# Kernel tuning notes

Measured on AMD Instinct MI355X. Metric: run time of the kernel, lower is better.

The kernel has to match this reference:

```python
import jax, jax.numpy as jnp
import numpy as np

B, L, D = 4, 2048, 1024
H, KD, VD = 16, 64, 64
EPS = 1e-5


def setup_inputs() -> dict:
    key = jax.random.key(0)
    ks = jax.random.split(key, 12)
    s_in = 1.0 / np.sqrt(D)
    s_out = 1.0 / np.sqrt(H * VD)
    return {
        "queries": jax.random.normal(ks[0], (B, L, D), dtype=jnp.float32),
        "Wq": jax.random.uniform(ks[1], (D, H * KD), jnp.float32, -s_in, s_in),
        "bq": jax.random.uniform(ks[2], (H * KD,), jnp.float32, -s_in, s_in),
        "Wk": jax.random.uniform(ks[3], (D, H * KD), jnp.float32, -s_in, s_in),
        "bk": jax.random.uniform(ks[4], (H * KD,), jnp.float32, -s_in, s_in),
        "Wv": jax.random.uniform(ks[5], (D, H * VD), jnp.float32, -s_in, s_in),
        "bv": jax.random.uniform(ks[6], (H * VD,), jnp.float32, -s_in, s_in),
        "Wo": jax.random.uniform(ks[7], (H * VD, D), jnp.float32, -s_out, s_out),
        "bo": jax.random.uniform(ks[8], (D,), jnp.float32, -s_out, s_out),
        "gamma": jnp.ones((D,), jnp.float32),
        "beta": jnp.zeros((D,), jnp.float32),
    }


def reference(queries, Wq, bq, Wk, bk, Wv, bv, Wo, bo, gamma, beta):
    # QKV projections -> [B, L, H, head_dim]
    q = (queries @ Wq + bq).reshape(B, L, H, KD)
    k = (queries @ Wk + bk).reshape(B, L, H, KD)
    v = (queries @ Wv + bv).reshape(B, L, H, VD)
    # scaled dot-product attention per head: scores [B, H, Lq, Lk]
    scores = jnp.einsum("bqhd,bkhd->bhqk", q, k) / np.sqrt(KD).astype(np.float32)
    attn = jax.nn.softmax(scores, axis=-1)
    out = jnp.einsum("bhqk,bkhd->bqhd", attn, v).reshape(B, L, H * VD)
    # out projection (dropout is identity in eval), residual + LayerNorm
    res = out @ Wo + bo + queries
    mu = jnp.mean(res, axis=-1, keepdims=True)
    var = jnp.var(res, axis=-1, keepdims=True)
    return (res - mu) / jnp.sqrt(var + EPS) * gamma + beta
```

## Files before the change

kernel.cpp:

```cpp
#include <hip/hip_runtime.h>
#include <hip/hip_bf16.h>

#define BATCH 4
#define SEQ   2048
#define DIM   1024
#define NHEAD 16
#define HDIM  64
#define EPS_LN 1e-5f
#define QSCALE 0.18033688011112042f

typedef __attribute__((ext_vector_type(8))) short short8;
typedef __attribute__((ext_vector_type(4))) float f32x4;

__device__ __forceinline__ unsigned short f2bf(float x) {
    __hip_bfloat16 h = __float2bfloat16(x);
    return *reinterpret_cast<unsigned short*>(&h);
}
__device__ __forceinline__ unsigned int pack2bf(float a, float b) {
    __hip_bfloat162 h = __float22bfloat162_rn(float2{a, b});
    return *reinterpret_cast<unsigned int*>(&h);
}

__device__ __forceinline__ void gl_lds16(const void* g, void* l) {
    __builtin_amdgcn_global_load_lds(
        (const __attribute__((address_space(1))) unsigned int*)g,
        (__attribute__((address_space(3))) unsigned int*)l,
        16, 0, 0);
}

__global__ __launch_bounds__(256) void prep_kernel(const float* __restrict__ W0,
                                                   const float* __restrict__ W1,
                                                   const float* __restrict__ W2,
                                                   const float* __restrict__ W3,
                                                   const float* __restrict__ queries,
                                                   unsigned short* __restrict__ Wqkvt,
                                                   unsigned short* __restrict__ Wot,
                                                   unsigned short* __restrict__ qout)
{
    const int z = blockIdx.z;
    const int t = threadIdx.x;

    if (z == 4) {
        const int nthr = 16 * 16 * 256;
        int i = (blockIdx.y * 16 + blockIdx.x) * 256 + t;
        for (int it = 0; it < (BATCH * SEQ * DIM / 4) / nthr; it++, i += nthr) {
            float4 v = ((const float4*)queries)[i];
            ushort4 u;
            u.x = f2bf(v.x); u.y = f2bf(v.y); u.z = f2bf(v.z); u.w = f2bf(v.w);
            ((ushort4*)qout)[i] = u;
        }
        return;
    }

    __shared__ float Ts[64][65];
    const float* W = (z == 0) ? W0 : (z == 1) ? W1 : (z == 2) ? W2 : W3;
    unsigned short* Wt = (z == 3) ? Wot : (Wqkvt + (size_t)z * DIM * DIM);

    const int k0 = blockIdx.y * 64, n0 = blockIdx.x * 64;
    const int lr = t >> 2, lq = t & 3;

#pragma unroll
    for (int i = 0; i < 4; i++) {
        float4 v = *(const float4*)(W + (size_t)(k0 + lr) * DIM + n0 + (lq * 4 + i) * 4);
        Ts[lr][(lq * 4 + i) * 4 + 0] = v.x;
        Ts[lr][(lq * 4 + i) * 4 + 1] = v.y;
        Ts[lr][(lq * 4 + i) * 4 + 2] = v.z;
        Ts[lr][(lq * 4 + i) * 4 + 3] = v.w;
    }
    __syncthreads();
#pragma unroll
    for (int i = 0; i < 4; i++) {
        const int c = lq * 16 + i * 4;
        ushort4 u;
        u.x = f2bf(Ts[c + 0][lr]);
        u.y = f2bf(Ts[c + 1][lr]);
        u.z = f2bf(Ts[c + 2][lr]);
        u.w = f2bf(Ts[c + 3][lr]);
        *(ushort4*)(Wt + (size_t)(n0 + lr) * DIM + k0 + c) = u;
    }
}

__global__ __launch_bounds__(256) void gemm_qkv(const unsigned short* __restrict__ A,
                                                const unsigned short* __restrict__ Bt,
                                                const float* __restrict__ bq,
                                                const float* __restrict__ bk,
                                                const float* __restrict__ bv,
                                                unsigned short* __restrict__ Qbf,
                                                unsigned short* __restrict__ Kbf,
                                                unsigned short* __restrict__ Vtb)
{
    __shared__ __attribute__((aligned(16))) unsigned short As[128 * 32];
    __shared__ __attribute__((aligned(16))) unsigned short Bs[128 * 32];

    const int tid = threadIdx.x;
    const int w = tid >> 6, lane = tid & 63;
    const int col = lane & 15, quad = lane >> 4;
    const int wm = (w >> 1) * 64, wn = (w & 1) * 64;
    const int m0 = blockIdx.y * 128, n0 = blockIdx.x * 128;

    f32x4 acc[4][4] = {};
    const int srow = tid >> 2, sc4 = tid & 3;

    for (int k0 = 0; k0 < DIM; k0 += 32) {
        __syncthreads();
#pragma unroll
        for (int it = 0; it < 2; it++) {
            gl_lds16(A  + (size_t)(m0 + srow + it * 64) * DIM + k0 + sc4 * 8,
                     (char*)As + w * 1024 + it * 4096);
            gl_lds16(Bt + (size_t)(n0 + srow + it * 64) * DIM + k0 + sc4 * 8,
                     (char*)Bs + w * 1024 + it * 4096);
        }
        __syncthreads();

        short8 af[4], bf[4];
#pragma unroll
        for (int mt = 0; mt < 4; mt++) af[mt] = *(short8*)&As[(wm + mt * 16 + col) * 32 + quad * 8];
#pragma unroll
        for (int nt = 0; nt < 4; nt++) bf[nt] = *(short8*)&Bs[(wn + nt * 16 + col) * 32 + quad * 8];

#pragma unroll
        for (int mt = 0; mt < 4; mt++)
#pragma unroll
            for (int nt = 0; nt < 4; nt++)
                acc[mt][nt] = __builtin_amdgcn_mfma_f32_16x16x32_bf16(af[mt], bf[nt], acc[mt][nt], 0, 0, 0);
    }

    const int sector = n0 >> 10;
    const float* bias = (sector == 0) ? bq : (sector == 1) ? bk : bv;

#pragma unroll
    for (int nt = 0; nt < 4; nt++) {
        const int n = n0 + wn + nt * 16 + col;
        const int nloc = n - (sector << 10);
        const float bvv = bias[nloc];
#pragma unroll
        for (int mt = 0; mt < 4; mt++) {
            const int mbase = m0 + wm + mt * 16 + quad * 4;
            if (sector == 0) {
#pragma unroll
                for (int r = 0; r < 4; r++)
                    Qbf[(size_t)(mbase + r) * DIM + nloc] = f2bf((acc[mt][nt][r] + bvv) * QSCALE);
            } else if (sector == 1) {
#pragma unroll
                for (int r = 0; r < 4; r++)
                    Kbf[(size_t)(mbase + r) * DIM + nloc] = f2bf(acc[mt][nt][r] + bvv);
            } else {
                const int h = nloc >> 6, d = nloc & 63;
                const int b = mbase >> 11, l = mbase & 2047;
                ushort4 u;
                u.x = f2bf(acc[mt][nt][0] + bvv);
                u.y = f2bf(acc[mt][nt][1] + bvv);
                u.z = f2bf(acc[mt][nt][2] + bvv);
                u.w = f2bf(acc[mt][nt][3] + bvv);
                *(ushort4*)(Vtb + ((size_t)((b * NHEAD + h) * HDIM + d)) * SEQ + l) = u;
            }
        }
    }
}

__global__ __launch_bounds__(256) void gemm_out(const unsigned short* __restrict__ A,
                                                const unsigned short* __restrict__ Bt,
                                                const float* __restrict__ bias,
                                                const float* __restrict__ resid,
                                                float* __restrict__ Cout)
{
    __shared__ __attribute__((aligned(16))) unsigned short As[128 * 32];
    __shared__ __attribute__((aligned(16))) unsigned short Bs[128 * 32];

    const int tid = threadIdx.x;
    const int w = tid >> 6, lane = tid & 63;
    const int col = lane & 15, quad = lane >> 4;
    const int wm = (w >> 1) * 64, wn = (w & 1) * 64;
    const int m0 = blockIdx.y * 128, n0 = blockIdx.x * 128;

    f32x4 acc[4][4] = {};
    const int srow = tid >> 2, sc4 = tid & 3;

    for (int k0 = 0; k0 < DIM; k0 += 32) {
        __syncthreads();
#pragma unroll
        for (int it = 0; it < 2; it++) {
            gl_lds16(A  + (size_t)(m0 + srow + it * 64) * DIM + k0 + sc4 * 8,
                     (char*)As + w * 1024 + it * 4096);
            gl_lds16(Bt + (size_t)(n0 + srow + it * 64) * DIM + k0 + sc4 * 8,
                     (char*)Bs + w * 1024 + it * 4096);
        }
        __syncthreads();

        short8 af[4], bf[4];
#pragma unroll
        for (int mt = 0; mt < 4; mt++) af[mt] = *(short8*)&As[(wm + mt * 16 + col) * 32 + quad * 8];
#pragma unroll
        for (int nt = 0; nt < 4; nt++) bf[nt] = *(short8*)&Bs[(wn + nt * 16 + col) * 32 + quad * 8];

#pragma unroll
        for (int mt = 0; mt < 4; mt++)
#pragma unroll
            for (int nt = 0; nt < 4; nt++)
                acc[mt][nt] = __builtin_amdgcn_mfma_f32_16x16x32_bf16(af[mt], bf[nt], acc[mt][nt], 0, 0, 0);
    }

#pragma unroll
    for (int nt = 0; nt < 4; nt++) {
        const int n = n0 + wn + nt * 16 + col;
        const float bvv = bias[n];
#pragma unroll
        for (int mt = 0; mt < 4; mt++) {
            const int mbase = m0 + wm + mt * 16 + quad * 4;
#pragma unroll
            for (int r = 0; r < 4; r++) {
                const size_t off = (size_t)(mbase + r) * DIM + n;
                Cout[off] = acc[mt][nt][r] + bvv + resid[off];
            }
        }
    }
}

#define KP 72
__global__ __launch_bounds__(256) void attn_mfma(const unsigned short* __restrict__ Qb,
                                                 const unsigned short* __restrict__ Kb,
                                                 const unsigned short* __restrict__ Vt,
                                                 unsigned short* __restrict__ Ob)
{
    __shared__ __attribute__((aligned(16))) unsigned short Ks[64 * KP];
    __shared__ __attribute__((aligned(16))) unsigned short Vs[64 * KP];
    __shared__ __attribute__((aligned(16))) unsigned short Ps[4][32 * KP];

    const int tid = threadIdx.x;
    const int w = tid >> 6, lane = tid & 63;
    const int col = lane & 15, quad = lane >> 4;

    const int bh  = blockIdx.x & 63;
    const int qt_ = blockIdx.x >> 6;
    const int b   = bh >> 4;
    const int h   = bh & 15;

    const int q0 = qt_ * 128 + w * 32;

    short8 qf[2][2];
#pragma unroll
    for (int qt = 0; qt < 2; qt++) {
        const size_t base = ((size_t)(b * SEQ) + q0 + qt * 16 + col) * DIM + h * HDIM + quad * 8;
        qf[qt][0] = *(const short8*)(Qb + base);
        qf[qt][1] = *(const short8*)(Qb + base + 32);
    }

    short8 onesf;
    {
        const short v = (col == 0) ? (short)0x3F80 : (short)0;
        onesf = short8{v, v, v, v, v, v, v, v};
    }

    f32x4 o[4][2] = {};
    f32x4 od[2]   = {};

    const size_t kbase0 = ((size_t)(b * SEQ)) * DIM + h * HDIM;
    const size_t vbase0 = ((size_t)((b * NHEAD + h) * HDIM)) * SEQ;

    const int srow = tid >> 3, sc = tid & 7;
    unsigned short* Pw = Ps[w];

    for (int kt = 0; kt < SEQ / 64; kt++) {
        __syncthreads();
#pragma unroll
        for (int it = 0; it < 2; it++) {
            const int row = srow + it * 32;
            *(int4*)&Ks[row * KP + sc * 8] = *(const int4*)(Kb + kbase0 + (size_t)(kt * 64 + row) * DIM + sc * 8);
            *(int4*)&Vs[row * KP + sc * 8] = *(const int4*)(Vt + vbase0 + (size_t)row * SEQ + kt * 64 + sc * 8);
        }
        __syncthreads();

#pragma unroll
        for (int nt = 0; nt < 4; nt++) {
            short8 kf0 = *(short8*)&Ks[(nt * 16 + col) * KP + quad * 8];
            short8 kf1 = *(short8*)&Ks[(nt * 16 + col) * KP + quad * 8 + 32];
#pragma unroll
            for (int qt = 0; qt < 2; qt++) {
                f32x4 s = {};
                s = __builtin_amdgcn_mfma_f32_16x16x32_bf16(kf0, qf[qt][0], s, 0, 0, 0);
                s = __builtin_amdgcn_mfma_f32_16x16x32_bf16(kf1, qf[qt][1], s, 0, 0, 0);
                const float p0 = __builtin_amdgcn_exp2f(s[0]);
                const float p1 = __builtin_amdgcn_exp2f(s[1]);
                const float p2 = __builtin_amdgcn_exp2f(s[2]);
                const float p3 = __builtin_amdgcn_exp2f(s[3]);
                uint2 pk;
                pk.x = pack2bf(p0, p1);
                pk.y = pack2bf(p2, p3);
                *(uint2*)&Pw[(qt * 16 + col) * KP + nt * 16 + quad * 4] = pk;
            }
        }

        short8 pf[2][2];
#pragma unroll
        for (int qt = 0; qt < 2; qt++) {
            pf[qt][0] = *(short8*)&Pw[(qt * 16 + col) * KP + quad * 8];
            pf[qt][1] = *(short8*)&Pw[(qt * 16 + col) * KP + quad * 8 + 32];
        }

#pragma unroll
        for (int qt = 0; qt < 2; qt++) {
            od[qt] = __builtin_amdgcn_mfma_f32_16x16x32_bf16(onesf, pf[qt][0], od[qt], 0, 0, 0);
            od[qt] = __builtin_amdgcn_mfma_f32_16x16x32_bf16(onesf, pf[qt][1], od[qt], 0, 0, 0);
        }

#pragma unroll
        for (int mt = 0; mt < 4; mt++) {
            short8 vf0 = *(short8*)&Vs[(mt * 16 + col) * KP + quad * 8];
            short8 vf1 = *(short8*)&Vs[(mt * 16 + col) * KP + quad * 8 + 32];
#pragma unroll
            for (int qt = 0; qt < 2; qt++) {
                o[mt][qt] = __builtin_amdgcn_mfma_f32_16x16x32_bf16(vf0, pf[qt][0], o[mt][qt], 0, 0, 0);
                o[mt][qt] = __builtin_amdgcn_mfma_f32_16x16x32_bf16(vf1, pf[qt][1], o[mt][qt], 0, 0, 0);
            }
        }
    }

#pragma unroll
    for (int qt = 0; qt < 2; qt++) {
        const float den = __shfl(od[qt][0], col);
        const float inv = 1.f / den;
        const size_t rowoff = ((size_t)(b * SEQ) + q0 + qt * 16 + col) * DIM + h * HDIM;
#pragma unroll
        for (int mt = 0; mt < 4; mt++) {
            ushort4 u;
            u.x = f2bf(o[mt][qt][0] * inv);
            u.y = f2bf(o[mt][qt][1] * inv);
            u.z = f2bf(o[mt][qt][2] * inv);
            u.w = f2bf(o[mt][qt][3] * inv);
            *(ushort4*)(Ob + rowoff + mt * 16 + quad * 4) = u;
        }
    }
}

__global__ __launch_bounds__(256) void layernorm_kernel(float* __restrict__ res,
                                                        const float* __restrict__ gamma,
                                                        const float* __restrict__ beta)
{
    const int tid = threadIdx.x;
    const int row = blockIdx.x;
    float4 xv = ((const float4*)(res + (size_t)row * DIM))[tid];

    float s  = xv.x + xv.y + xv.z + xv.w;
    float sq = xv.x * xv.x + xv.y * xv.y + xv.z * xv.z + xv.w * xv.w;
#pragma unroll
    for (int off = 32; off; off >>= 1) {
        s  += __shfl_xor(s, off);
        sq += __shfl_xor(sq, off);
    }
    __shared__ float sm[8];
    const int w = tid >> 6, lane = tid & 63;
    if (lane == 0) { sm[w] = s; sm[4 + w] = sq; }
    __syncthreads();
    const float st  = sm[0] + sm[1] + sm[2] + sm[3];
    const float sqt = sm[4] + sm[5] + sm[6] + sm[7];
    const float mu   = st * (1.f / DIM);
    const float var  = sqt * (1.f / DIM) - mu * mu;
    const float rstd = rsqrtf(var + EPS_LN);

    float4 g  = ((const float4*)gamma)[tid];
    float4 be = ((const float4*)beta)[tid];
    float4 o;
    o.x = (xv.x - mu) * rstd * g.x + be.x;
    o.y = (xv.y - mu) * rstd * g.y + be.y;
    o.z = (xv.z - mu) * rstd * g.z + be.z;
    o.w = (xv.w - mu) * rstd * g.w + be.w;
    ((float4*)(res + (size_t)row * DIM))[tid] = o;
}

extern "C" void kernel_launch(void* const* d_in, const int* in_sizes, int n_in,
                              void* d_out, int out_size, void* d_ws, size_t ws_size,
                              hipStream_t stream)
{
    const float* queries = (const float*)d_in[0];
    const float* Wq = (const float*)d_in[1];
    const float* bq = (const float*)d_in[2];
    const float* Wk = (const float*)d_in[3];
    const float* bk = (const float*)d_in[4];
    const float* Wv = (const float*)d_in[5];
    const float* bv = (const float*)d_in[6];
    const float* Wo = (const float*)d_in[7];
    const float* bo = (const float*)d_in[8];
    const float* gamma = (const float*)d_in[9];
    const float* beta  = (const float*)d_in[10];
    float* outp = (float*)d_out;

    const int M = BATCH * SEQ;
    const size_t BUF = (size_t)M * DIM;
    const size_t WSZ = (size_t)DIM * DIM;

    unsigned short* w0  = (unsigned short*)d_ws;
    unsigned short* qin = w0;
    unsigned short* Qbf = w0 + BUF;
    unsigned short* Kbf = w0 + 2 * BUF;
    unsigned short* Vtb = w0 + 3 * BUF;
    unsigned short* Wqkvt = w0 + 4 * BUF;
    unsigned short* Wot   = Wqkvt + 3 * WSZ;
    unsigned short* Obf = qin;

    dim3 blk(256);

    dim3 pgrid(DIM / 64, DIM / 64, 5);
    prep_kernel<<<pgrid, blk, 0, stream>>>(Wq, Wk, Wv, Wo, queries, Wqkvt, Wot, qin);

    dim3 qkvgrid(3 * DIM / 128, M / 128);
    gemm_qkv<<<qkvgrid, blk, 0, stream>>>(qin, Wqkvt, bq, bk, bv, Qbf, Kbf, Vtb);

    attn_mfma<<<BATCH * NHEAD * (SEQ / 128), blk, 0, stream>>>(Qbf, Kbf, Vtb, Obf);

    dim3 ogrid(DIM / 128, M / 128);
    gemm_out<<<ogrid, blk, 0, stream>>>(Obf, Wot, bo, queries, outp);

    layernorm_kernel<<<M, blk, 0, stream>>>(outp, gamma, beta);
}
```

Measured before the change: 319.1 us.

## Register-prefetch K/V tiles and shuffle P via permlane swaps instead of LDS

Measured after the change: 377.0 us. 18.2% more time.

```diff
diff --git a/kernel.cpp b/kernel.cpp
--- a/kernel.cpp
+++ b/kernel.cpp
@@ -19,6 +19,13 @@
 __device__ __forceinline__ unsigned int pack2bf(float a, float b) {
     __hip_bfloat162 h = __float22bfloat162_rn(float2{a, b});
     return *reinterpret_cast<unsigned int*>(&h);
+}
+
+__device__ __forceinline__ void pl32_swap(unsigned& a, unsigned& b) {
+    asm("v_permlane32_swap_b32 %0, %1" : "+v"(a), "+v"(b));
+}
+__device__ __forceinline__ void pl16_swap(unsigned& a, unsigned& b) {
+    asm("v_permlane16_swap_b32 %0, %1" : "+v"(a), "+v"(b));
 }
 
 __device__ __forceinline__ void gl_lds16(const void* g, void* l) {
@@ -217,14 +224,13 @@
 }
 
 #define KP 72
-__global__ __launch_bounds__(256) void attn_mfma(const unsigned short* __restrict__ Qb,
-                                                 const unsigned short* __restrict__ Kb,
-                                                 const unsigned short* __restrict__ Vt,
-                                                 unsigned short* __restrict__ Ob)
+__global__ __launch_bounds__(256, 4) void attn_mfma(const unsigned short* __restrict__ Qb,
+                                                    const unsigned short* __restrict__ Kb,
+                                                    const unsigned short* __restrict__ Vt,
+                                                    unsigned short* __restrict__ Ob)
 {
     __shared__ __attribute__((aligned(16))) unsigned short Ks[64 * KP];
     __shared__ __attribute__((aligned(16))) unsigned short Vs[64 * KP];
-    __shared__ __attribute__((aligned(16))) unsigned short Ps[4][32 * KP];
 
     const int tid = threadIdx.x;
     const int w = tid >> 6, lane = tid & 63;
@@ -258,43 +264,65 @@
     const size_t vbase0 = ((size_t)((b * NHEAD + h) * HDIM)) * SEQ;
 
     const int srow = tid >> 3, sc = tid & 7;
-    unsigned short* Pw = Ps[w];
+
+    int4 kr[2], vr[2];
+#pragma unroll
+    for (int it = 0; it < 2; it++) {
+        const int row = srow + it * 32;
+        kr[it] = *(const int4*)(Kb + kbase0 + (size_t)row * DIM + sc * 8);
+        vr[it] = *(const int4*)(Vt + vbase0 + (size_t)row * SEQ + sc * 8);
+    }
 
     for (int kt = 0; kt < SEQ / 64; kt++) {
         __syncthreads();
 #pragma unroll
         for (int it = 0; it < 2; it++) {
             const int row = srow + it * 32;
-            *(int4*)&Ks[row * KP + sc * 8] = *(const int4*)(Kb + kbase0 + (size_t)(kt * 64 + row) * DIM + sc * 8);
-            *(int4*)&Vs[row * KP + sc * 8] = *(const int4*)(Vt + vbase0 + (size_t)row * SEQ + kt * 64 + sc * 8);
-        }
-        __syncthreads();
-
-#pragma unroll
-        for (int nt = 0; nt < 4; nt++) {
-            short8 kf0 = *(short8*)&Ks[(nt * 16 + col) * KP + quad * 8];
-            short8 kf1 = *(short8*)&Ks[(nt * 16 + col) * KP + quad * 8 + 32];
+            *(int4*)&Ks[row * KP + sc * 8] = kr[it];
+            *(int4*)&Vs[row * KP + sc * 8] = vr[it];
+        }
+        if (kt + 1 < SEQ / 64) {
+#pragma unroll
+            for (int it = 0; it < 2; it++) {
+                const int row = srow + it * 32;
+                kr[it] = *(const int4*)(Kb + kbase0 + (size_t)((kt + 1) * 64 + row) * DIM + sc * 8);
+                vr[it] = *(const int4*)(Vt + vbase0 + (size_t)row * SEQ + (kt + 1) * 64 + sc * 8);
+            }
+        }
+        __syncthreads();
+
+        short8 pf[2][2];
+#pragma unroll
+        for (int f = 0; f < 2; f++) {
+            unsigned pa[2][2], pb[2][2];
+#pragma unroll
+            for (int ntl = 0; ntl < 2; ntl++) {
+                const int nt = f * 2 + ntl;
+                short8 kf0 = *(short8*)&Ks[(nt * 16 + col) * KP + quad * 8];
+                short8 kf1 = *(short8*)&Ks[(nt * 16 + col) * KP + quad * 8 + 32];
+#pragma unroll
+                for (int qt = 0; qt < 2; qt++) {
+                    f32x4 s = {};
+                    s = __builtin_amdgcn_mfma_f32_16x16x32_bf16(kf0, qf[qt][0], s, 0, 0, 0);
+                    s = __builtin_amdgcn_mfma_f32_16x16x32_bf16(kf1, qf[qt][1], s, 0, 0, 0);
+                    pa[qt][ntl] = pack2bf(__builtin_amdgcn_exp2f(s[0]),
+                                          __builtin_amdgcn_exp2f(s[1]));
+                    pb[qt][ntl] = pack2bf(__builtin_amdgcn_exp2f(s[2]),
+                                          __builtin_amdgcn_exp2f(s[3]));
+                }
+            }
 #pragma unroll
             for (int qt = 0; qt < 2; qt++) {
-                f32x4 s = {};
-                s = __builtin_amdgcn_mfma_f32_16x16x32_bf16(kf0, qf[qt][0], s, 0, 0, 0);
-                s = __builtin_amdgcn_mfma_f32_16x16x32_bf16(kf1, qf[qt][1], s, 0, 0, 0);
-                const float p0 = __builtin_amdgcn_exp2f(s[0]);
-                const float p1 = __builtin_amdgcn_exp2f(s[1]);
-                const float p2 = __builtin_amdgcn_exp2f(s[2]);
-                const float p3 = __builtin_amdgcn_exp2f(s[3]);
-                uint2 pk;
-                pk.x = pack2bf(p0, p1);
-                pk.y = pack2bf(p2, p3);
-                *(uint2*)&Pw[(qt * 16 + col) * KP + nt * 16 + quad * 4] = pk;
-            }
-        }
-
-        short8 pf[2][2];
-#pragma unroll
-        for (int qt = 0; qt < 2; qt++) {
-            pf[qt][0] = *(short8*)&Pw[(qt * 16 + col) * KP + quad * 8];
-            pf[qt][1] = *(short8*)&Pw[(qt * 16 + col) * KP + quad * 8 + 32];
+                unsigned a0 = pa[qt][0], a1 = pa[qt][1];
+                unsigned b0 = pb[qt][0], b1 = pb[qt][1];
+                pl32_swap(a0, a1);
+                pl32_swap(b0, b1);
+                pl16_swap(a0, a1);
+                pl16_swap(b0, b1);
+                union { unsigned u[4]; short8 s8; } c;
+                c.u[0] = a0; c.u[1] = b0; c.u[2] = a1; c.u[3] = b1;
+                pf[qt][f] = c.s8;
+            }
         }
 
 #pragma unroll
```
